# Kernel optimization log

Hardware: AMD Instinct MI355X
Metric: run time of the kernel (lower is better)

The kernel has to match this reference:

```python
import jax, jax.numpy as jnp
import numpy as np

B, L, E = 16, 1022, 1280
D, H, FF, NL = 512, 8, 2048, 4
DH = D // H
EPS = 1e-5


def layer_norm(x, s, b):
    m = jnp.mean(x, axis=-1, keepdims=True)
    v = jnp.mean(jnp.square(x - m), axis=-1, keepdims=True)
    return (x - m) * jax.lax.rsqrt(v + EPS) * s + b


def setup_inputs() -> dict:
    key = jax.random.key(0)
    ks = jax.random.split(key, 12)
    s = 0.02
    return {
        "embeddings": jax.random.normal(ks[0], (B, L, E), jnp.float32),
        "mask": jnp.ones((B, L), jnp.float32),
        "position": jnp.tile(jnp.arange(L, dtype=jnp.int32)[None, :], (B, 1)),
        "proj_w": jax.random.normal(ks[1], (D, E), jnp.float32) * s,
        "proj_b": jnp.zeros((D,), jnp.float32),
        "proj_ln_s": jnp.ones((D,), jnp.float32),
        "proj_ln_b": jnp.zeros((D,), jnp.float32),
        "ln1_s": jnp.ones((NL, D), jnp.float32),
        "ln1_b": jnp.zeros((NL, D), jnp.float32),
        "in_w": jax.random.normal(ks[2], (NL, 3 * D, D), jnp.float32) * s,
        "in_b": jnp.zeros((NL, 3 * D), jnp.float32),
        "out_w": jax.random.normal(ks[3], (NL, D, D), jnp.float32) * s,
        "out_b": jnp.zeros((NL, D), jnp.float32),
        "ln2_s": jnp.ones((NL, D), jnp.float32),
        "ln2_b": jnp.zeros((NL, D), jnp.float32),
        "w1": jax.random.normal(ks[4], (NL, FF, D), jnp.float32) * s,
        "b1": jnp.zeros((NL, FF), jnp.float32),
        "w2": jax.random.normal(ks[5], (NL, D, FF), jnp.float32) * s,
        "b2": jnp.zeros((NL, D), jnp.float32),
        "h1_w": jax.random.normal(ks[6], (128, 2 * D), jnp.float32) * s,
        "h1_b": jnp.zeros((128,), jnp.float32),
        "hln_s": jnp.ones((128,), jnp.float32),
        "hln_b": jnp.zeros((128,), jnp.float32),
        "h2_w": jax.random.normal(ks[7], (1, 128), jnp.float32) * s,
        "h2_b": jnp.zeros((1,), jnp.float32),
    }


def _rope_tables():
    inv_freq = 1.0 / (10000.0 ** (jnp.arange(0, DH, 2, dtype=jnp.float32) / DH))
    t = jnp.arange(L, dtype=jnp.float32)
    freqs = jnp.outer(t, inv_freq)          # [L, DH/2]
    emb = jnp.concatenate([freqs, freqs], axis=-1)  # [L, DH]
    return jnp.cos(emb), jnp.sin(emb)


def _rotate_half(x):
    x1, x2 = jnp.split(x, 2, axis=-1)
    return jnp.concatenate([-x2, x1], axis=-1)


def _apply_rope(x, cos, sin):
    # x: [B, L, D] -> per-head rotation -> [B, L, D]
    xh = x.reshape(B, L, H, DH)
    xh = xh * cos[None, :, None, :] + _rotate_half(xh) * sin[None, :, None, :]
    return xh.reshape(B, L, D)


def _forward(embeddings, mask, proj_w, proj_b, proj_ln_s, proj_ln_b,
             ln1_s, ln1_b, in_w, in_b, out_w, out_b, ln2_s, ln2_b,
             w1, b1, w2, b2, h1_w, h1_b, hln_s, hln_b, h2_w, h2_b):
    cos, sin = _rope_tables()
    x = layer_norm(embeddings @ proj_w.T + proj_b, proj_ln_s, proj_ln_b)  # [B,L,D]
    pad = mask <= 0  # True where padded (~mask.bool())
    scale = 1.0 / jnp.sqrt(jnp.float32(DH))
    for i in range(NL):
        n = layer_norm(x, ln1_s[i], ln1_b[i])
        q_in = _apply_rope(n, cos, sin)
        k_in = _apply_rope(n, cos, sin)
        v_in = n
        wq, wk, wv = jnp.split(in_w[i], 3, axis=0)
        bq, bk, bv = jnp.split(in_b[i], 3, axis=0)
        qh = (q_in @ wq.T + bq).reshape(B, L, H, DH)
        kh = (k_in @ wk.T + bk).reshape(B, L, H, DH)
        vh = (v_in @ wv.T + bv).reshape(B, L, H, DH)
        scores = jnp.einsum('blhd,bmhd->bhlm', qh, kh) * scale
        scores = jnp.where(pad[:, None, None, :], jnp.float32(-1e9), scores)
        attn = jax.nn.softmax(scores, axis=-1)
        o = jnp.einsum('bhlm,bmhd->blhd', attn, vh).reshape(B, L, D)
        x = x + (o @ out_w[i].T + out_b[i])
        n2 = layer_norm(x, ln2_s[i], ln2_b[i])
        x = x + (jax.nn.relu(n2 @ w1[i].T + b1[i]) @ w2[i].T + b2[i])
    # masked mean pool
    gctx = (x * mask[..., None]).sum(axis=1) / mask.sum(axis=1, keepdims=True)  # [B,D]
    combined = jnp.concatenate([x, jnp.broadcast_to(gctx[:, None, :], (B, L, D))], axis=-1)
    h = jax.nn.relu(layer_norm(combined @ h1_w.T + h1_b, hln_s, hln_b))
    logits = (h @ h2_w.T + h2_b).squeeze(-1)  # [B,L]
    return logits


def reference(embeddings, mask, position, proj_w, proj_b, proj_ln_s, proj_ln_b,
              ln1_s, ln1_b, in_w, in_b, out_w, out_b, ln2_s, ln2_b,
              w1, b1, w2, b2, h1_w, h1_b, hln_s, hln_b, h2_w, h2_b):
    # position is accepted for API parity but unused (as in the torch module)
    return _forward(embeddings, mask, proj_w, proj_b, proj_ln_s, proj_ln_b,
                    ln1_s, ln1_b, in_w, in_b, out_w, out_b, ln2_s, ln2_b,
                    w1, b1, w2, b2, h1_w, h1_b, hln_s, hln_b, h2_w, h2_b)
```

## Files before the change

### kernel.cpp

```cpp
#include <hip/hip_runtime.h>
#include <cstdint>
#include <cstddef>

#define B_   16
#define L_   1022
#define E_   1280
#define D_   512
#define H_   8
#define FF_  2048
#define NL_  4
#define DH_  64
#define BL_  (B_*L_)
#define EPS_ 1e-5f
#define QSC_ 0.18033688011112042f

typedef unsigned short u16;
typedef unsigned int   u32;
typedef unsigned long long u64;
typedef float f32x4 __attribute__((ext_vector_type(4)));
typedef short s16x8 __attribute__((ext_vector_type(8)));
typedef u32 u32x4 __attribute__((ext_vector_type(4)));

__device__ __forceinline__ u16 f2bf(float f) {
    u32 u = __builtin_bit_cast(u32, f);
    u += 0x7fffu + ((u >> 16) & 1u);
    return (u16)(u >> 16);
}
__device__ __forceinline__ float bf2f(u16 u) {
    return __builtin_bit_cast(float, (u32)u << 16);
}
__device__ __forceinline__ u32 pack2bf(float a, float b) {
    return (u32)f2bf(a) | ((u32)f2bf(b) << 16);
}

__global__ __launch_bounds__(256)
void cast_k(const float* __restrict__ src, u16* __restrict__ dst, int n8) {
    int t = blockIdx.x * 256 + threadIdx.x;
    if (t >= n8) return;
    const float* s = src + (size_t)t * 8;
    float4 a = *(const float4*)(s);
    float4 b = *(const float4*)(s + 4);
    s16x8 o;
    o[0] = (short)f2bf(a.x); o[1] = (short)f2bf(a.y);
    o[2] = (short)f2bf(a.z); o[3] = (short)f2bf(a.w);
    o[4] = (short)f2bf(b.x); o[5] = (short)f2bf(b.y);
    o[6] = (short)f2bf(b.z); o[7] = (short)f2bf(b.w);
    *(s16x8*)(dst + (size_t)t * 8) = o;
}

__global__ __launch_bounds__(256)
void castq_k(const float* __restrict__ src, u16* __restrict__ dst, int n8) {
    int t = blockIdx.x * 256 + threadIdx.x;
    if (t >= n8) return;
    int row = t >> 6;
    float sc = (row % 1536) < 512 ? QSC_ : 1.0f;
    const float* s = src + (size_t)t * 8;
    float4 a = *(const float4*)(s);
    float4 b = *(const float4*)(s + 4);
    s16x8 o;
    o[0] = (short)f2bf(a.x * sc); o[1] = (short)f2bf(a.y * sc);
    o[2] = (short)f2bf(a.z * sc); o[3] = (short)f2bf(a.w * sc);
    o[4] = (short)f2bf(b.x * sc); o[5] = (short)f2bf(b.y * sc);
    o[6] = (short)f2bf(b.z * sc); o[7] = (short)f2bf(b.w * sc);
    *(s16x8*)(dst + (size_t)t * 8) = o;
}

__global__ __launch_bounds__(256)
void qbias_k(const float* __restrict__ ib, float* __restrict__ qbs) {
    int t = blockIdx.x * 256 + threadIdx.x;
    if (t >= NL_ * 1024) return;
    int i = t >> 10, j = t & 1023;
    float sc = j < 512 ? QSC_ : 1.0f;
    qbs[t] = ib[i * 1536 + j] * sc;
}

__global__ __launch_bounds__(256)
void h1cast_k(const float* __restrict__ src, u16* __restrict__ dst) {
    int t = blockIdx.x * 256 + threadIdx.x;
    if (t >= 128 * 512 / 8) return;
    int row = t >> 6, c8 = (t & 63) << 3;
    const float* s = src + (size_t)row * 1024 + c8;
    float4 a = *(const float4*)(s);
    float4 b = *(const float4*)(s + 4);
    s16x8 o;
    o[0] = (short)f2bf(a.x); o[1] = (short)f2bf(a.y);
    o[2] = (short)f2bf(a.z); o[3] = (short)f2bf(a.w);
    o[4] = (short)f2bf(b.x); o[5] = (short)f2bf(b.y);
    o[6] = (short)f2bf(b.z); o[7] = (short)f2bf(b.w);
    *(s16x8*)(dst + (size_t)row * 512 + c8) = o;
}

__global__ void tables_k(float* __restrict__ ct, float* __restrict__ st) {
    int idx = blockIdx.x * blockDim.x + threadIdx.x;
    if (idx >= L_ * DH_) return;
    int l = idx / DH_;
    int d = idx % DH_;
    int j = d & 31;
    float invf = powf(10000.0f, -(float)(2 * j) / (float)DH_);
    float ang = (float)l * invf;
    ct[idx] = cosf(ang);
    st[idx] = sinf(ang);
}

template<bool RELU, bool RESID, bool OUTBF, bool ROWBIAS>
__global__ __launch_bounds__(256)
void mgemm_k(const u16* __restrict__ A, const u16* __restrict__ W,
             const float* __restrict__ bias, const u16* __restrict__ resid,
             void* __restrict__ Cout, int M, int N, int K)
{
    constexpr int LDT = 72;
    __shared__ u16 As[128 * LDT];
    __shared__ u16 Ws[128 * LDT];
    const int nt = N >> 7;
    const int bx = blockIdx.x % nt;
    const int by = blockIdx.x / nt;
    const int m0 = by << 7, n0 = bx << 7;
    const int tid = threadIdx.x;
    const int lane = tid & 63, wid = tid >> 6;
    const int wr = wid >> 1, wc = wid & 1;
    const int lr = lane & 15, lk = lane >> 4;

    f32x4 acc[4][4];
#pragma unroll
    for (int m = 0; m < 4; m++)
#pragma unroll
        for (int n = 0; n < 4; n++) acc[m][n] = (f32x4)0.0f;

    for (int k0 = 0; k0 < K; k0 += 64) {
        s16x8 va[4], vw[4];
#pragma unroll
        for (int u = 0; u < 4; u++) {
            int ch = tid + (u << 8);
            int r = ch >> 3, c8 = (ch & 7) << 3;
            int ar = m0 + r; if (ar >= M) ar = M - 1;
            va[u] = *(const s16x8*)(A + (size_t)ar * K + k0 + c8);
            vw[u] = *(const s16x8*)(W + (size_t)(n0 + r) * K + k0 + c8);
        }
        __syncthreads();
#pragma unroll
        for (int u = 0; u < 4; u++) {
            int ch = tid + (u << 8);
            int r = ch >> 3, c8 = (ch & 7) << 3;
            *(s16x8*)&As[r * LDT + c8] = va[u];
            *(s16x8*)&Ws[r * LDT + c8] = vw[u];
        }
        __syncthreads();
#pragma unroll
        for (int kk = 0; kk < 2; kk++) {
            s16x8 af[4], bf[4];
#pragma unroll
            for (int m = 0; m < 4; m++)
                af[m] = *(const s16x8*)&As[(wr * 64 + m * 16 + lr) * LDT + kk * 32 + lk * 8];
#pragma unroll
            for (int n = 0; n < 4; n++)
                bf[n] = *(const s16x8*)&Ws[(wc * 64 + n * 16 + lr) * LDT + kk * 32 + lk * 8];
#pragma unroll
            for (int m = 0; m < 4; m++)
#pragma unroll
                for (int n = 0; n < 4; n++)
                    acc[m][n] = __builtin_amdgcn_mfma_f32_16x16x32_bf16(
                        af[m], bf[n], acc[m][n], 0, 0, 0);
        }
    }

    float bv[4];
    if constexpr (!ROWBIAS) {
#pragma unroll
        for (int n = 0; n < 4; n++) bv[n] = bias[n0 + wc * 64 + n * 16 + lr];
    }
#pragma unroll
    for (int m = 0; m < 4; m++) {
#pragma unroll
        for (int j = 0; j < 4; j++) {
            int row = m0 + wr * 64 + m * 16 + lk * 4 + j;
            if (row >= M) continue;
            const float* rb = nullptr;
            if constexpr (ROWBIAS) rb = bias + (size_t)(row / L_) * N;
#pragma unroll
            for (int n = 0; n < 4; n++) {
                int col = n0 + wc * 64 + n * 16 + lr;
                float c = acc[m][n][j];
                if constexpr (ROWBIAS) c += rb[col];
                else                   c += bv[n];
                if constexpr (RELU) c = fmaxf(c, 0.0f);
                if constexpr (RESID) c += bf2f(resid[(size_t)row * N + col]);
                if constexpr (OUTBF) ((u16*)Cout)[(size_t)row * N + col] = f2bf(c);
                else                 ((float*)Cout)[(size_t)row * N + col] = c;
            }
        }
    }
}

template<int DD, bool RELU, bool OUTBF, bool INBF>
__global__ __launch_bounds__(256)
void ln_k(const void* __restrict__ xin, const float* __restrict__ s,
          const float* __restrict__ bb, void* __restrict__ out, int M)
{
    const int lane = threadIdx.x & 63;
    const int row = (blockIdx.x << 2) + (threadIdx.x >> 6);
    if (row >= M) return;
    constexpr int NV = DD / 64;
    float v[NV];
    if constexpr (INBF) {
        const u16* xr = (const u16*)xin + (size_t)row * DD;
        if constexpr (NV == 8) {
            s16x8 t = *(const s16x8*)(xr + lane * 8);
#pragma unroll
            for (int e = 0; e < 8; e++) v[e] = bf2f((u16)t[e]);
        } else {
            v[0] = bf2f(xr[lane * 2]); v[1] = bf2f(xr[lane * 2 + 1]);
        }
    } else {
        const float* xr = (const float*)xin + (size_t)row * DD;
        if constexpr (NV == 8) {
            *(float4*)(v)     = *(const float4*)(xr + lane * 8);
            *(float4*)(v + 4) = *(const float4*)(xr + lane * 8 + 4);
        } else {
            float2 t = *(const float2*)(xr + lane * 2);
            v[0] = t.x; v[1] = t.y;
        }
    }
    float sum = 0.f, sq = 0.f;
#pragma unroll
    for (int e = 0; e < NV; e++) { sum += v[e]; sq += v[e] * v[e]; }
#pragma unroll
    for (int msk = 1; msk < 64; msk <<= 1) {
        sum += __shfl_xor(sum, msk);
        sq  += __shfl_xor(sq, msk);
    }
    const float mean = sum * (1.0f / DD);
    const float var  = sq * (1.0f / DD) - mean * mean;
    const float rstd = rsqrtf(var + EPS_);
#pragma unroll
    for (int e = 0; e < NV; e++) {
        int d = lane * NV + e;
        float r = (v[e] - mean) * rstd * s[d] + bb[d];
        if constexpr (RELU) r = fmaxf(r, 0.0f);
        v[e] = r;
    }
    if constexpr (OUTBF) {
        u16* orow = (u16*)out + (size_t)row * DD;
        if constexpr (NV == 8) {
            s16x8 o;
#pragma unroll
            for (int e = 0; e < 8; e++) o[e] = (short)f2bf(v[e]);
            *(s16x8*)(orow + lane * 8) = o;
        } else {
            orow[lane * 2] = f2bf(v[0]); orow[lane * 2 + 1] = f2bf(v[1]);
        }
    } else {
        float* orow = (float*)out + (size_t)row * DD;
        if constexpr (NV == 8) {
            *(float4*)(orow + lane * 8)     = *(float4*)(v);
            *(float4*)(orow + lane * 8 + 4) = *(float4*)(v + 4);
        } else {
            float2 t; t.x = v[0]; t.y = v[1];
            *(float2*)(orow + lane * 2) = t;
        }
    }
}

__global__ __launch_bounds__(256)
void rope_k(const u16* __restrict__ n, const float* __restrict__ ct,
            const float* __restrict__ st, u16* __restrict__ r)
{
    int t = blockIdx.x * 256 + threadIdx.x;
    if (t >= BL_ * D_ / 8) return;
    int idx = t << 3;
    int l = (idx / D_) % L_;
    int d = idx & (D_ - 1);
    int dd = d & 63;
    s16x8 xv = *(const s16x8*)(n + idx);
    int pidx; float sgn;
    if (dd < 32) { pidx = idx + 32; sgn = -1.0f; }
    else         { pidx = idx - 32; sgn =  1.0f; }
    s16x8 pv = *(const s16x8*)(n + pidx);
    float4 c0 = *(const float4*)(ct + l * DH_ + dd);
    float4 c1 = *(const float4*)(ct + l * DH_ + dd + 4);
    float4 s0 = *(const float4*)(st + l * DH_ + dd);
    float4 s1 = *(const float4*)(st + l * DH_ + dd + 4);
    float cc[8] = {c0.x,c0.y,c0.z,c0.w,c1.x,c1.y,c1.z,c1.w};
    float ss[8] = {s0.x,s0.y,s0.z,s0.w,s1.x,s1.y,s1.z,s1.w};
    s16x8 o;
#pragma unroll
    for (int e = 0; e < 8; e++) {
        float xf = bf2f((u16)xv[e]);
        float pf = bf2f((u16)pv[e]);
        o[e] = (short)f2bf(xf * cc[e] + sgn * pf * ss[e]);
    }
    *(s16x8*)(r + idx) = o;
}

__global__ __launch_bounds__(256)
void attn_k(const u16* __restrict__ qk, const u16* __restrict__ v,
            const float* __restrict__ mask, u16* __restrict__ o)
{
    constexpr int LDA = 68;
    __shared__ u16 Kt[64 * LDA];
    __shared__ u16 Vt[64 * LDA];
    const int bh = blockIdx.x >> 4, qt = blockIdx.x & 15;
    const int b = bh >> 3, h = bh & 7;
    const int tid = threadIdx.x;
    const int lane = tid & 63, w = tid >> 6;
    const int lr = lane & 15, lg = lane >> 4;
    const size_t basebl = (size_t)b * L_;

    const int qrow = qt * 64 + w * 16 + lr;
    const int qc = qrow < L_ ? qrow : L_ - 1;
    s16x8 bq[2];
#pragma unroll
    for (int kk = 0; kk < 2; kk++)
        bq[kk] = *(const s16x8*)(qk + (basebl + qc) * 1024 + h * DH_ + kk * 32 + lg * 8);

    f32x4 oacc[4];
#pragma unroll
    for (int n = 0; n < 4; n++) oacc[n] = (f32x4)0.0f;
    float m_run = -1e30f, l_run = 0.f;

    const int st_key = tid >> 3;
    const int st_d8 = (tid & 7) << 3;
    const int src0 = lr + ((lane & 16) << 1);
    const int src1 = src0 + 16;
    const bool ahi = (lg >> 1) != 0;

    for (int kt = 0; kt < 16; kt++) {
        __syncthreads();
#pragma unroll
        for (int u = 0; u < 2; u++) {
            int key = st_key + u * 32;
            int gk = kt * 64 + key; if (gk >= L_) gk = L_ - 1;
            s16x8 kv = *(const s16x8*)(qk + (basebl + gk) * 1024 + 512 + h * DH_ + st_d8);
            s16x8 vv = *(const s16x8*)(v  + (basebl + gk) * D_ + h * DH_ + st_d8);
            *(s16x8*)&Kt[key * LDA + st_d8] = kv;
#pragma unroll
            for (int e = 0; e < 8; e++) Vt[(st_d8 + e) * LDA + key] = (u16)vv[e];
        }
        __syncthreads();

        int gkey = kt * 64 + lane;
        bool vb = (gkey < L_) && (mask[basebl + gkey] > 0.0f);
        u64 vm = __ballot(vb);

        f32x4 sacc[4];
#pragma unroll
        for (int n = 0; n < 4; n++) {
            sacc[n] = (f32x4)0.0f;
#pragma unroll
            for (int kk = 0; kk < 2; kk++) {
                s16x8 ak = *(const s16x8*)&Kt[(n * 16 + lr) * LDA + kk * 32 + lg * 8];
                sacc[n] = __builtin_amdgcn_mfma_f32_16x16x32_bf16(ak, bq[kk], sacc[n], 0, 0, 0);
            }
        }

        float p[4][4];
        float tm = -1e30f;
#pragma unroll
        for (int n = 0; n < 4; n++)
#pragma unroll
            for (int j = 0; j < 4; j++) {
                int kl = 16 * n + 4 * lg + j;
                float s = ((vm >> kl) & 1ull) ? sacc[n][j] : -1e30f;
                p[n][j] = s;
                tm = fmaxf(tm, s);
            }
        tm = fmaxf(tm, __shfl_xor(tm, 16));
        tm = fmaxf(tm, __shfl_xor(tm, 32));
        float nm = fmaxf(m_run, tm);
        float corr = exp2f(m_run - nm);
        m_run = nm;
        float ts = 0.f;
#pragma unroll
        for (int n = 0; n < 4; n++)
#pragma unroll
            for (int j = 0; j < 4; j++) {
                p[n][j] = exp2f(p[n][j] - nm);
                ts += p[n][j];
            }
        ts += __shfl_xor(ts, 16);
        ts += __shfl_xor(ts, 32);
        l_run = l_run * corr + ts;
#pragma unroll
        for (int n = 0; n < 4; n++) oacc[n] *= corr;

        u32 pk[4][2];
#pragma unroll
        for (int n = 0; n < 4; n++) {
            pk[n][0] = pack2bf(p[n][0], p[n][1]);
            pk[n][1] = pack2bf(p[n][2], p[n][3]);
        }
        u32 r0[4][2], r1[4][2];
#pragma unroll
        for (int n = 0; n < 4; n++)
#pragma unroll
            for (int i = 0; i < 2; i++) {
                r0[n][i] = (u32)__shfl((int)pk[n][i], src0);
                r1[n][i] = (u32)__shfl((int)pk[n][i], src1);
            }
#pragma unroll
        for (int kk = 0; kk < 2; kk++) {
            u32x4 bw;
            bw[0] = ahi ? r0[2 * kk + 1][0] : r0[2 * kk][0];
            bw[1] = ahi ? r0[2 * kk + 1][1] : r0[2 * kk][1];
            bw[2] = ahi ? r1[2 * kk + 1][0] : r1[2 * kk][0];
            bw[3] = ahi ? r1[2 * kk + 1][1] : r1[2 * kk][1];
            s16x8 bp = __builtin_bit_cast(s16x8, bw);
#pragma unroll
            for (int n2 = 0; n2 < 4; n2++) {
                s16x8 av = *(const s16x8*)&Vt[(n2 * 16 + lr) * LDA + kk * 32 + lg * 8];
                oacc[n2] = __builtin_amdgcn_mfma_f32_16x16x32_bf16(av, bp, oacc[n2], 0, 0, 0);
            }
        }
    }

    __syncthreads();
    u16* Ol = &Kt[w * 16 * LDA];
    float inv = 1.0f / l_run;
#pragma unroll
    for (int n = 0; n < 4; n++)
#pragma unroll
        for (int j = 0; j < 4; j++)
            Ol[lr * LDA + 16 * n + 4 * lg + j] = f2bf(oacc[n][j] * inv);
    int orow = lane >> 2, oc = (lane & 3) * 16;
    int qg = qt * 64 + w * 16 + orow;
    if (qg < L_) {
        s16x8 o0 = *(const s16x8*)&Ol[orow * LDA + oc];
        s16x8 o1 = *(const s16x8*)&Ol[orow * LDA + oc + 8];
        *(s16x8*)(o + (basebl + qg) * D_ + h * DH_ + oc) = o0;
        *(s16x8*)(o + (basebl + qg) * D_ + h * DH_ + oc + 8) = o1;
    }
}

__global__ __launch_bounds__(512)
void pool1_k(const u16* __restrict__ x, const float* __restrict__ mask,
             float* __restrict__ pp, float* __restrict__ mp)
{
    const int b = blockIdx.x, sp = blockIdx.y;
    const int d = threadIdx.x;
    const int l0 = sp * 64;
    float acc = 0.f;
    for (int l = l0; l < l0 + 64 && l < L_; l++)
        acc += bf2f(x[((size_t)b * L_ + l) * D_ + d]) * mask[b * L_ + l];
    pp[((size_t)b * 16 + sp) * D_ + d] = acc;
    if (d == 0) {
        float ms = 0.f;
        for (int l = l0; l < l0 + 64 && l < L_; l++) ms += mask[b * L_ + l];
        mp[b * 16 + sp] = ms;
    }
}

__global__ __launch_bounds__(512)
void pool2_k(const float* __restrict__ pp, const float* __restrict__ mp,
             float* __restrict__ g)
{
    const int b = blockIdx.x;
    const int d = threadIdx.x;
    float acc = 0.f, ms = 0.f;
#pragma unroll
    for (int sp = 0; sp < 16; sp++) {
        acc += pp[((size_t)b * 16 + sp) * D_ + d];
        ms += mp[b * 16 + sp];
    }
    g[b * D_ + d] = acc / ms;
}

__global__ __launch_bounds__(256)
void gpart_k(const float* __restrict__ g, const float* __restrict__ h1w,
             const float* __restrict__ h1b, float* __restrict__ gp)
{
    const int lane = threadIdx.x & 63;
    const int gid = (blockIdx.x << 2) + (threadIdx.x >> 6);
    const int b = gid >> 7, j = gid & 127;
    const float* wr = h1w + (size_t)j * (2 * D_) + D_;
    const float* gr = g + b * D_;
    float4 a0 = *(const float4*)(gr + lane * 8);
    float4 a1 = *(const float4*)(gr + lane * 8 + 4);
    float4 w0 = *(const float4*)(wr + lane * 8);
    float4 w1v = *(const float4*)(wr + lane * 8 + 4);
    float acc = a0.x * w0.x + a0.y * w0.y + a0.z * w0.z + a0.w * w0.w
              + a1.x * w1v.x + a1.y * w1v.y + a1.z * w1v.z + a1.w * w1v.w;
#pragma unroll
    for (int msk = 1; msk < 64; msk <<= 1) acc += __shfl_xor(acc, msk);
    if (lane == 0) gp[b * 128 + j] = acc + h1b[j];
}

__global__ __launch_bounds__(256)
void logits_k(const float* __restrict__ h, const float* __restrict__ w,
              const float* __restrict__ bsc, float* __restrict__ out, int M)
{
    const int lane = threadIdx.x & 63;
    const int row = (blockIdx.x << 2) + (threadIdx.x >> 6);
    if (row >= M) return;
    float2 hv = *(const float2*)(h + (size_t)row * 128 + lane * 2);
    float2 wv = *(const float2*)(w + lane * 2);
    float acc = hv.x * wv.x + hv.y * wv.y;
#pragma unroll
    for (int msk = 1; msk < 64; msk <<= 1) acc += __shfl_xor(acc, msk);
    if (lane == 0) out[row] = acc + bsc[0];
}

extern "C" void kernel_launch(void* const* d_in, const int* in_sizes, int n_in,
                              void* d_out, int out_size, void* d_ws, size_t ws_size,
                              hipStream_t stream)
{
    const float* emb       = (const float*)d_in[0];
    const float* mask      = (const float*)d_in[1];
    const float* proj_w    = (const float*)d_in[3];
    const float* proj_b    = (const float*)d_in[4];
    const float* proj_ln_s = (const float*)d_in[5];
    const float* proj_ln_b = (const float*)d_in[6];
    const float* ln1_s     = (const float*)d_in[7];
    const float* ln1_b     = (const float*)d_in[8];
    const float* in_w      = (const float*)d_in[9];
    const float* in_b      = (const float*)d_in[10];
    const float* out_w     = (const float*)d_in[11];
    const float* out_b     = (const float*)d_in[12];
    const float* ln2_s     = (const float*)d_in[13];
    const float* ln2_b     = (const float*)d_in[14];
    const float* w1        = (const float*)d_in[15];
    const float* b1        = (const float*)d_in[16];
    const float* w2        = (const float*)d_in[17];
    const float* b2        = (const float*)d_in[18];
    const float* h1_w      = (const float*)d_in[19];
    const float* h1_b      = (const float*)d_in[20];
    const float* hln_s     = (const float*)d_in[21];
    const float* hln_b     = (const float*)d_in[22];
    const float* h2_w      = (const float*)d_in[23];
    const float* h2_b      = (const float*)d_in[24];
    float* out = (float*)d_out;

    float* ws = (float*)d_ws;
    const size_t S = (size_t)BL_ * D_;
    u16* X = (u16*)ws;
    float* Rf = ws + S;
    u16* QKB   = (u16*)(ws + S);
    u16* VB    = (u16*)(ws + 2 * S);
    u16* NbB   = (u16*)(ws + 2 * S) + S;
    u16* FFb16 = (u16*)(ws + 3 * S);
    u16* RopeB = FFb16;
    u16* embB  = FFb16;
    u16* RB    = (u16*)(ws + 4 * S);
    u16* projwB = (u16*)(ws + 5 * S);
    u16* iwB  = projwB + 512 * 1280;
    u16* owB  = iwB + (size_t)NL_ * 3 * D_ * D_;
    u16* w1B  = owB + (size_t)NL_ * D_ * D_;
    u16* w2B  = w1B + (size_t)NL_ * FF_ * D_;
    u16* h1wB = w2B + (size_t)NL_ * D_ * FF_;
    float* CT = ws + 5 * S + 6651904;
    float* ST = CT + L_ * DH_;
    float* GC = ST + L_ * DH_;
    float* GP = GC + B_ * D_;
    float* Pp = GP + B_ * 128;
    float* Mp = Pp + (size_t)B_ * 16 * D_;
    float* QBS = Mp + B_ * 16;
    float* Hb = Rf;

    const int MT = 128;
    const dim3 blk(256);
    const int lnGrid = (BL_ + 3) / 4;

    cast_k<<<(BL_ * E_ / 8 + 255) / 256, blk, 0, stream>>>(emb, embB, BL_ * E_ / 8);
    cast_k<<<(512 * 1280 / 8 + 255) / 256, blk, 0, stream>>>(proj_w, projwB, 512 * 1280 / 8);
    castq_k<<<(NL_ * 3 * D_ * D_ / 8 + 255) / 256, blk, 0, stream>>>(in_w, iwB, NL_ * 3 * D_ * D_ / 8);
    qbias_k<<<(NL_ * 1024 + 255) / 256, blk, 0, stream>>>(in_b, QBS);
    cast_k<<<(NL_ * D_ * D_ / 8 + 255) / 256, blk, 0, stream>>>(out_w, owB, NL_ * D_ * D_ / 8);
    cast_k<<<(NL_ * FF_ * D_ / 8 + 255) / 256, blk, 0, stream>>>(w1, w1B, NL_ * FF_ * D_ / 8);
    cast_k<<<(NL_ * D_ * FF_ / 8 + 255) / 256, blk, 0, stream>>>(w2, w2B, NL_ * D_ * FF_ / 8);
    h1cast_k<<<(128 * 512 / 8 + 255) / 256, blk, 0, stream>>>(h1_w, h1wB);
    tables_k<<<(L_ * DH_ + 255) / 256, blk, 0, stream>>>(CT, ST);

    mgemm_k<false,false,false,false><<<MT * (D_ / 128), blk, 0, stream>>>(
        embB, projwB, proj_b, nullptr, Rf, BL_, D_, E_);
    ln_k<D_,false,true,false><<<lnGrid, blk, 0, stream>>>(Rf, proj_ln_s, proj_ln_b, X, BL_);

    for (int i = 0; i < NL_; i++) {
        const u16* iw = iwB + (size_t)i * 3 * D_ * D_;
        const float* ib = in_b + (size_t)i * 3 * D_;
        ln_k<D_,false,true,true><<<lnGrid, blk, 0, stream>>>(X, ln1_s + i * D_, ln1_b + i * D_, NbB, BL_);
        mgemm_k<false,false,true,false><<<MT * 4, blk, 0, stream>>>(
            NbB, iw + 2 * D_ * D_, ib + 2 * D_, nullptr, VB, BL_, D_, D_);
        rope_k<<<(BL_ * D_ / 8 + 255) / 256, blk, 0, stream>>>(NbB, CT, ST, RopeB);
        mgemm_k<false,false,true,false><<<MT * 8, blk, 0, stream>>>(
            RopeB, iw, QBS + (size_t)i * 1024, nullptr, QKB, BL_, 1024, D_);
        attn_k<<<B_ * H_ * 16, blk, 0, stream>>>(QKB, VB, mask, RB);
        mgemm_k<false,true,true,false><<<MT * 4, blk, 0, stream>>>(
            RB, owB + (size_t)i * D_ * D_, out_b + i * D_, X, X, BL_, D_, D_);
        ln_k<D_,false,true,true><<<lnGrid, blk, 0, stream>>>(X, ln2_s + i * D_, ln2_b + i * D_, NbB, BL_);
        mgemm_k<true,false,true,false><<<MT * 16, blk, 0, stream>>>(
            NbB, w1B + (size_t)i * FF_ * D_, b1 + i * FF_, nullptr, FFb16, BL_, FF_, D_);
        mgemm_k<false,true,true,false><<<MT * 4, blk, 0, stream>>>(
            FFb16, w2B + (size_t)i * D_ * FF_, b2 + i * D_, X, X, BL_, D_, FF_);
    }

    pool1_k<<<dim3(B_, 16), dim3(512), 0, stream>>>(X, mask, Pp, Mp);
    pool2_k<<<B_, dim3(512), 0, stream>>>(Pp, Mp, GC);
    gpart_k<<<(B_ * 128) / 4, blk, 0, stream>>>(GC, h1_w, h1_b, GP);
    mgemm_k<false,false,false,true><<<MT * 1, blk, 0, stream>>>(
        X, h1wB, GP, nullptr, Hb, BL_, 128, D_);
    ln_k<128,true,false,false><<<lnGrid, blk, 0, stream>>>(Hb, hln_s, hln_b, Hb, BL_);
    logits_k<<<lnGrid, blk, 0, stream>>>(Hb, h2_w, h2_b, out, BL_);
}
```

Before: 1.450 ms.

## Use 8-wave GEMM blocks and fuse RoPE into the pre-attention layernorm

The bf16 MFMA GEMM now runs 512 threads per block, with each wave computing a 64x32 sub-tile instead of 64x64. This halves per-thread accumulators and global load work and is meant to raise the number of resident waves and hide latency better. RoPE is folded into the LN1 kernel using a lane shuffle for the rotate-half partner, removing a separate kernel launch and one bf16 re-read of the normalized activations. The fused RoPE works on fp32 values before they are rounded to bf16, which slightly changes numerics. Each wave now does less MFMA work per shared-memory fragment load.

Result: faster. 1.413 ms (-2.6%).

```diff
diff --git a/kernel.cpp b/kernel.cpp
--- a/kernel.cpp
+++ b/kernel.cpp
@@ -103,7 +103,7 @@
 }
 
 template<bool RELU, bool RESID, bool OUTBF, bool ROWBIAS>
-__global__ __launch_bounds__(256)
+__global__ __launch_bounds__(512)
 void mgemm_k(const u16* __restrict__ A, const u16* __restrict__ W,
              const float* __restrict__ bias, const u16* __restrict__ resid,
              void* __restrict__ Cout, int M, int N, int K)
@@ -117,20 +117,20 @@
     const int m0 = by << 7, n0 = bx << 7;
     const int tid = threadIdx.x;
     const int lane = tid & 63, wid = tid >> 6;
-    const int wr = wid >> 1, wc = wid & 1;
+    const int wr = wid >> 2, wc = wid & 3;
     const int lr = lane & 15, lk = lane >> 4;
 
-    f32x4 acc[4][4];
+    f32x4 acc[4][2];
 #pragma unroll
     for (int m = 0; m < 4; m++)
 #pragma unroll
-        for (int n = 0; n < 4; n++) acc[m][n] = (f32x4)0.0f;
+        for (int n = 0; n < 2; n++) acc[m][n] = (f32x4)0.0f;
 
     for (int k0 = 0; k0 < K; k0 += 64) {
-        s16x8 va[4], vw[4];
-#pragma unroll
-        for (int u = 0; u < 4; u++) {
-            int ch = tid + (u << 8);
+        s16x8 va[2], vw[2];
+#pragma unroll
+        for (int u = 0; u < 2; u++) {
+            int ch = tid + (u << 9);
             int r = ch >> 3, c8 = (ch & 7) << 3;
             int ar = m0 + r; if (ar >= M) ar = M - 1;
             va[u] = *(const s16x8*)(A + (size_t)ar * K + k0 + c8);
@@ -138,8 +138,8 @@
         }
         __syncthreads();
 #pragma unroll
-        for (int u = 0; u < 4; u++) {
-            int ch = tid + (u << 8);
+        for (int u = 0; u < 2; u++) {
+            int ch = tid + (u << 9);
             int r = ch >> 3, c8 = (ch & 7) << 3;
             *(s16x8*)&As[r * LDT + c8] = va[u];
             *(s16x8*)&Ws[r * LDT + c8] = vw[u];
@@ -147,26 +147,26 @@
         __syncthreads();
 #pragma unroll
         for (int kk = 0; kk < 2; kk++) {
-            s16x8 af[4], bf[4];
+            s16x8 af[4], bf[2];
 #pragma unroll
             for (int m = 0; m < 4; m++)
                 af[m] = *(const s16x8*)&As[(wr * 64 + m * 16 + lr) * LDT + kk * 32 + lk * 8];
 #pragma unroll
-            for (int n = 0; n < 4; n++)
-                bf[n] = *(const s16x8*)&Ws[(wc * 64 + n * 16 + lr) * LDT + kk * 32 + lk * 8];
+            for (int n = 0; n < 2; n++)
+                bf[n] = *(const s16x8*)&Ws[(wc * 32 + n * 16 + lr) * LDT + kk * 32 + lk * 8];
 #pragma unroll
             for (int m = 0; m < 4; m++)
 #pragma unroll
-                for (int n = 0; n < 4; n++)
+                for (int n = 0; n < 2; n++)
                     acc[m][n] = __builtin_amdgcn_mfma_f32_16x16x32_bf16(
                         af[m], bf[n], acc[m][n], 0, 0, 0);
         }
     }
 
-    float bv[4];
+    float bv[2];
     if constexpr (!ROWBIAS) {
 #pragma unroll
-        for (int n = 0; n < 4; n++) bv[n] = bias[n0 + wc * 64 + n * 16 + lr];
+        for (int n = 0; n < 2; n++) bv[n] = bias[n0 + wc * 32 + n * 16 + lr];
     }
 #pragma unroll
     for (int m = 0; m < 4; m++) {
@@ -177,8 +177,8 @@
             const float* rb = nullptr;
             if constexpr (ROWBIAS) rb = bias + (size_t)(row / L_) * N;
 #pragma unroll
-            for (int n = 0; n < 4; n++) {
-                int col = n0 + wc * 64 + n * 16 + lr;
+            for (int n = 0; n < 2; n++) {
+                int col = n0 + wc * 32 + n * 16 + lr;
                 float c = acc[m][n][j];
                 if constexpr (ROWBIAS) c += rb[col];
                 else                   c += bv[n];
@@ -191,10 +191,13 @@
     }
 }
 
-template<int DD, bool RELU, bool OUTBF, bool INBF>
+template<int DD, bool RELU, bool OUTBF, bool INBF, bool ROPE>
 __global__ __launch_bounds__(256)
 void ln_k(const void* __restrict__ xin, const float* __restrict__ s,
-          const float* __restrict__ bb, void* __restrict__ out, int M)
+          const float* __restrict__ bb, void* __restrict__ out, int M,
+          const float* __restrict__ ct = nullptr,
+          const float* __restrict__ st = nullptr,
+          u16* __restrict__ rout = nullptr)
 {
     const int lane = threadIdx.x & 63;
     const int row = (blockIdx.x << 2) + (threadIdx.x >> 6);
@@ -258,37 +261,25 @@
             *(float2*)(orow + lane * 2) = t;
         }
     }
-}
-
-__global__ __launch_bounds__(256)
-void rope_k(const u16* __restrict__ n, const float* __restrict__ ct,
-            const float* __restrict__ st, u16* __restrict__ r)
-{
-    int t = blockIdx.x * 256 + threadIdx.x;
-    if (t >= BL_ * D_ / 8) return;
-    int idx = t << 3;
-    int l = (idx / D_) % L_;
-    int d = idx & (D_ - 1);
-    int dd = d & 63;
-    s16x8 xv = *(const s16x8*)(n + idx);
-    int pidx; float sgn;
-    if (dd < 32) { pidx = idx + 32; sgn = -1.0f; }
-    else         { pidx = idx - 32; sgn =  1.0f; }
-    s16x8 pv = *(const s16x8*)(n + pidx);
-    float4 c0 = *(const float4*)(ct + l * DH_ + dd);
-    float4 c1 = *(const float4*)(ct + l * DH_ + dd + 4);
-    float4 s0 = *(const float4*)(st + l * DH_ + dd);
-    float4 s1 = *(const float4*)(st + l * DH_ + dd + 4);
-    float cc[8] = {c0.x,c0.y,c0.z,c0.w,c1.x,c1.y,c1.z,c1.w};
-    float ss[8] = {s0.x,s0.y,s0.z,s0.w,s1.x,s1.y,s1.z,s1.w};
-    s16x8 o;
-#pragma unroll
-    for (int e = 0; e < 8; e++) {
-        float xf = bf2f((u16)xv[e]);
-        float pf = bf2f((u16)pv[e]);
-        o[e] = (short)f2bf(xf * cc[e] + sgn * pf * ss[e]);
-    }
-    *(s16x8*)(r + idx) = o;
+    if constexpr (ROPE) {
+        float pv[8];
+#pragma unroll
+        for (int e = 0; e < 8; e++) pv[e] = __shfl_xor(v[e], 4);
+        const int l = row % L_;
+        const int dd0 = (lane & 7) * 8;
+        const float sgn = (lane & 4) ? 1.0f : -1.0f;
+        float4 c0 = *(const float4*)(ct + l * DH_ + dd0);
+        float4 c1 = *(const float4*)(ct + l * DH_ + dd0 + 4);
+        float4 s0 = *(const float4*)(st + l * DH_ + dd0);
+        float4 s1 = *(const float4*)(st + l * DH_ + dd0 + 4);
+        float cc[8] = {c0.x,c0.y,c0.z,c0.w,c1.x,c1.y,c1.z,c1.w};
+        float ss[8] = {s0.x,s0.y,s0.z,s0.w,s1.x,s1.y,s1.z,s1.w};
+        s16x8 ro;
+#pragma unroll
+        for (int e = 0; e < 8; e++)
+            ro[e] = (short)f2bf(v[e] * cc[e] + sgn * pv[e] * ss[e]);
+        *(s16x8*)(rout + (size_t)row * DD + lane * 8) = ro;
+    }
 }
 
 __global__ __launch_bounds__(256)
@@ -556,6 +547,7 @@
 
     const int MT = 128;
     const dim3 blk(256);
+    const dim3 gblk(512);
     const int lnGrid = (BL_ + 3) / 4;
 
     cast_k<<<(BL_ * E_ / 8 + 255) / 256, blk, 0, stream>>>(emb, embB, BL_ * E_ / 8);
@@ -568,34 +560,35 @@
     h1cast_k<<<(128 * 512 / 8 + 255) / 256, blk, 0, stream>>>(h1_w, h1wB);
     tables_k<<<(L_ * DH_ + 255) / 256, blk, 0, stream>>>(CT, ST);
 
-    mgemm_k<false,false,false,false><<<MT * (D_ / 128), blk, 0, stream>>>(
+    mgemm_k<false,false,false,false><<<MT * (D_ / 128), gblk, 0, stream>>>(
         embB, projwB, proj_b, nullptr, Rf, BL_, D_, E_);
-    ln_k<D_,false,true,false><<<lnGrid, blk, 0, stream>>>(Rf, proj_ln_s, proj_ln_b, X, BL_);
+    ln_k<D_,false,true,false,false><<<lnGrid, blk, 0, stream>>>(Rf, proj_ln_s, proj_ln_b, X, BL_);
 
     for (int i = 0; i < NL_; i++) {
         const u16* iw = iwB + (size_t)i * 3 * D_ * D_;
         const float* ib = in_b + (size_t)i * 3 * D_;
-        ln_k<D_,false,true,true><<<lnGrid, blk, 0, stream>>>(X, ln1_s + i * D_, ln1_b + i * D_, NbB, BL_);
-        mgemm_k<false,false,true,false><<<MT * 4, blk, 0, stream>>>(
+        ln_k<D_,false,true,true,true><<<lnGrid, blk, 0, stream>>>(
+            X, ln1_s + i * D_, ln1_b + i * D_, NbB, BL_, CT, ST, RopeB);
+        mgemm_k<false,false,true,false><<<MT * 4, gblk, 0, stream>>>(
             NbB, iw + 2 * D_ * D_, ib + 2 * D_, nullptr, VB, BL_, D_, D_);
-        rope_k<<<(BL_ * D_ / 8 + 255) / 256, blk, 0, stream>>>(NbB, CT, ST, RopeB);
-        mgemm_k<false,false,true,false><<<MT * 8, blk, 0, stream>>>(
+        mgemm_k<false,false,true,false><<<MT * 8, gblk, 0, stream>>>(
             RopeB, iw, QBS + (size_t)i * 1024, nullptr, QKB, BL_, 1024, D_);
         attn_k<<<B_ * H_ * 16, blk, 0, stream>>>(QKB, VB, mask, RB);
-        mgemm_k<false,true,true,false><<<MT * 4, blk, 0, stream>>>(
+        mgemm_k<false,true,true,false><<<MT * 4, gblk, 0, stream>>>(
             RB, owB + (size_t)i * D_ * D_, out_b + i * D_, X, X, BL_, D_, D_);
-        ln_k<D_,false,true,true><<<lnGrid, blk, 0, stream>>>(X, ln2_s + i * D_, ln2_b + i * D_, NbB, BL_);
-        mgemm_k<true,false,true,false><<<MT * 16, blk, 0, stream>>>(
+        ln_k<D_,false,true,true,false><<<lnGrid, blk, 0, stream>>>(
+            X, ln2_s + i * D_, ln2_b + i * D_, NbB, BL_);
+        mgemm_k<true,false,true,false><<<MT * 16, gblk, 0, stream>>>(
             NbB, w1B + (size_t)i * FF_ * D_, b1 + i * FF_, nullptr, FFb16, BL_, FF_, D_);
-        mgemm_k<false,true,true,false><<<MT * 4, blk, 0, stream>>>(
+        mgemm_k<false,true,true,false><<<MT * 4, gblk, 0, stream>>>(
             FFb16, w2B + (size_t)i * D_ * FF_, b2 + i * D_, X, X, BL_, D_, FF_);
     }
 
     pool1_k<<<dim3(B_, 16), dim3(512), 0, stream>>>(X, mask, Pp, Mp);
     pool2_k<<<B_, dim3(512), 0, stream>>>(Pp, Mp, GC);
     gpart_k<<<(B_ * 128) / 4, blk, 0, stream>>>(GC, h1_w, h1_b, GP);
-    mgemm_k<false,false,false,true><<<MT * 1, blk, 0, stream>>>(
+    mgemm_k<false,false,false,true><<<MT * 1, gblk, 0, stream>>>(
         X, h1wB, GP, nullptr, Hb, BL_, 128, D_);
-    ln_k<128,true,false,false><<<lnGrid, blk, 0, stream>>>(Hb, hln_s, hln_b, Hb, BL_);
+    ln_k<128,true,false,false,false><<<lnGrid, blk, 0, stream>>>(Hb, hln_s, hln_b, Hb, BL_);
     logits_k<<<lnGrid, blk, 0, stream>>>(Hb, h2_w, h2_b, out, BL_);
 }
```
